# Performance work log

Hardware: AMD Instinct MI355X
Metric: run time of the kernel (lower is better)

The kernel has to match this reference:

```python
import jax, jax.numpy as jnp
import numpy as np

NUM_TOKENS = 8192
MODEL_DIM = 4096
NUM_EXPERTS = 64
CAPACITY_FACTOR = 1.0


def setup_inputs() -> dict:
    key = jax.random.key(0)
    k1, k2 = jax.random.split(key)
    inp = jax.random.normal(k1, (NUM_TOKENS, MODEL_DIM), dtype=jnp.float32)
    wg = jax.random.normal(k2, (NUM_EXPERTS, MODEL_DIM), dtype=jnp.float32) * (1.0 / np.sqrt(MODEL_DIM))
    return {"input": inp, "wg_weight": wg}


def reference(input, wg_weight):
    # logits = input @ wg.T  -> [T, E]
    logits = jnp.einsum('td,ed->te', input, wg_weight)
    num_tokens, num_experts = logits.shape
    capacity = int(CAPACITY_FACTOR * ((num_tokens + num_experts - 1) // num_experts))

    indices1_s = jnp.argmax(logits, axis=1)                      # [T]
    mask1 = jax.nn.one_hot(indices1_s, num_experts, dtype=logits.dtype)  # [T, E]
    gates = jax.nn.softmax(logits, axis=1)                       # [T, E]
    gates1_s = jnp.sum(gates * mask1, axis=1)                    # [T]

    # locations: position of each token within its chosen expert's queue
    # (exclusive cumsum over the one-hot mask, gathered at the chosen expert)
    locations1 = jnp.cumsum(mask1, axis=0) - 1.0                 # [T, E]
    locations1_s = jnp.sum(locations1 * mask1, axis=1).astype(jnp.int32)  # [T]

    # load-balancing aux loss (float32 branch of the original)
    me = jnp.sum(gates, axis=0)                                  # [E]
    ce = jnp.sum(mask1, axis=0)                                  # [E]
    l_aux = jnp.sum(me * ce) * (num_experts / (num_tokens * num_tokens))

    return (l_aux, indices1_s.astype(jnp.int32), locations1_s, gates1_s)
```

## Files before the change

### kernel.cpp

```cpp
#include <hip/hip_runtime.h>

namespace {
constexpr int TOK = 8192;
constexpr int DIM = 4096;
constexpr int NE  = 64;
constexpr int TB  = 128;
constexpr int KS  = 8;
constexpr int KR  = DIM / KS;
constexpr int NKS = KR / 32;
constexpr int TOTKS = DIM / 32;
constexpr int NT  = TOK / TB;
constexpr int GB  = 64;
constexpr int NCH = TOK / GB;
}

typedef _Float16 f16x8 __attribute__((ext_vector_type(8)));
typedef float    f32x4 __attribute__((ext_vector_type(4)));

__global__ __launch_bounds__(256) void prepack_w(
    const float* __restrict__ W, f16x8* __restrict__ whi,
    f16x8* __restrict__ wlo) {
  const int gid = blockIdx.x * 256 + threadIdx.x;
  const int lane = gid & 63;
  const int gk   = (gid >> 6) & (TOTKS - 1);
  const int et   = gid >> 13;
  const int e = et * 16 + (lane & 15);
  const int k = gk * 32 + (lane >> 4) * 8;
  const float4 r0 = *(const float4*)(W + (size_t)e * DIM + k);
  const float4 r1 = *(const float4*)(W + (size_t)e * DIM + k + 4);
  f16x8 hi, lo;
  const float rv[8] = {r0.x, r0.y, r0.z, r0.w, r1.x, r1.y, r1.z, r1.w};
#pragma unroll
  for (int j = 0; j < 8; ++j) {
    const _Float16 h = (_Float16)rv[j];
    hi[j] = h;
    lo[j] = (_Float16)(rv[j] - (float)h);
  }
  whi[gid] = hi;
  wlo[gid] = lo;
}

__global__ __launch_bounds__(512, 4) void gemm_split(
    const float* __restrict__ A, const f16x8* __restrict__ whi,
    const f16x8* __restrict__ wlo, float* __restrict__ partial) {
  const int bid  = blockIdx.x;
  const int tile = bid & (NT - 1);
  const int ks   = bid / NT;
  const int t0   = tile * TB;
  const int tid  = threadIdx.x;
  const int w    = tid >> 6;
  const int lane = tid & 63;
  const int col  = lane & 15;
  const int quad = lane >> 4;

  const float* Ap = A + (size_t)(t0 + w * 16 + col) * DIM + ks * KR + quad * 8;
  const int gk0 = ks * NKS;

  f32x4 acc[4];
#pragma unroll
  for (int et = 0; et < 4; ++et) acc[et] = (f32x4)0.0f;

  float4 a0  = *(const float4*)(Ap);
  float4 a1  = *(const float4*)(Ap + 4);
  float4 a0n = *(const float4*)(Ap + 32);
  float4 a1n = *(const float4*)(Ap + 36);
  f16x8 bh[4], bl[4];
#pragma unroll
  for (int et = 0; et < 4; ++et) {
    const size_t bi = ((size_t)(et * TOTKS + gk0) << 6) + lane;
    bh[et] = whi[bi];
    bl[et] = wlo[bi];
  }

  for (int it = 0; it < NKS; ++it) {
    f16x8 bhn[4], bln[4];
    if (it + 1 < NKS) {
#pragma unroll
      for (int et = 0; et < 4; ++et) {
        const size_t bi = ((size_t)(et * TOTKS + gk0 + it + 1) << 6) + lane;
        bhn[et] = whi[bi];
        bln[et] = wlo[bi];
      }
    }
    float4 a0nn, a1nn;
    if (it + 2 < NKS) {
      a0nn = *(const float4*)(Ap + (it + 2) * 32);
      a1nn = *(const float4*)(Ap + (it + 2) * 32 + 4);
    }
    const float av[8] = {a0.x, a0.y, a0.z, a0.w, a1.x, a1.y, a1.z, a1.w};
    f16x8 ah, al;
#pragma unroll
    for (int j = 0; j < 8; ++j) {
      const _Float16 h = (_Float16)av[j];
      ah[j] = h;
      al[j] = (_Float16)(av[j] - (float)h);
    }
#pragma unroll
    for (int et = 0; et < 4; ++et) {
      acc[et] = __builtin_amdgcn_mfma_f32_16x16x32_f16(ah, bh[et], acc[et], 0, 0, 0);
      acc[et] = __builtin_amdgcn_mfma_f32_16x16x32_f16(ah, bl[et], acc[et], 0, 0, 0);
      acc[et] = __builtin_amdgcn_mfma_f32_16x16x32_f16(al, bh[et], acc[et], 0, 0, 0);
    }
    a0 = a0n; a1 = a1n; a0n = a0nn; a1n = a1nn;
#pragma unroll
    for (int et = 0; et < 4; ++et) { bh[et] = bhn[et]; bl[et] = bln[et]; }
  }

  float* P = partial + (size_t)ks * TOK * NE;
  const int tb = t0 + w * 16 + quad * 4;
#pragma unroll
  for (int et = 0; et < 4; ++et) {
    const int e = et * 16 + col;
#pragma unroll
    for (int r = 0; r < 4; ++r)
      P[(size_t)(tb + r) * NE + e] = acc[et][r];
  }
}

__global__ __launch_bounds__(256) void gating(
    const float* __restrict__ partial, float* __restrict__ out,
    int* __restrict__ idx_int, int* __restrict__ rankp,
    int* __restrict__ hist, float* __restrict__ me_part) {
  __shared__ float L[GB * 65];
  __shared__ float mx[GB];
  __shared__ float dninv[GB];
  __shared__ int   eid[GB];
  const int b = blockIdx.x, tid = threadIdx.x;
  const size_t base = (size_t)b * GB * NE;

#pragma unroll
  for (int j = 0; j < (GB * NE) / 256; ++j) {
    const int idx = tid + 256 * j;
    float s = 0.0f;
#pragma unroll
    for (int k = 0; k < KS; ++k)
      s += partial[(size_t)k * TOK * NE + base + idx];
    L[(idx >> 6) * 65 + (idx & 63)] = s;
  }
  __syncthreads();

  if (tid < GB) {
    const int t = tid;
    float m = -3.0e38f; int bi = 0;
    for (int e = 0; e < NE; ++e) {
      const float v = L[t * 65 + e];
      if (v > m) { m = v; bi = e; }
    }
    float s = 0.0f;
    for (int e = 0; e < NE; ++e) s += __expf(L[t * 65 + e] - m);
    const float inv = 1.0f / s;
    mx[t] = m; dninv[t] = inv; eid[t] = bi;
    const int gt = b * GB + t;
    out[1 + gt]           = (float)bi;
    out[1 + 2 * TOK + gt] = inv;
    idx_int[gt] = bi;
  }
  __syncthreads();

  if (tid < GB) {
    const int t = tid, e = eid[t];
    int r = 0;
    for (int j = 0; j < t; ++j) r += (eid[j] == e) ? 1 : 0;
    rankp[b * GB + t] = r;
    int c = 0;
    for (int t2 = 0; t2 < GB; ++t2) c += (eid[t2] == tid) ? 1 : 0;
    hist[b * NE + tid] = c;
  } else if (tid < 2 * GB) {
    const int e = tid - GB;
    float s = 0.0f;
    for (int t2 = 0; t2 < GB; ++t2)
      s += __expf(L[t2 * 65 + e] - mx[t2]) * dninv[t2];
    me_part[b * NE + e] = s;
  }
}

__global__ __launch_bounds__(256) void finalize(
    const int* __restrict__ idx_int, const int* __restrict__ rankp,
    const int* __restrict__ hist, const float* __restrict__ me_part,
    float* __restrict__ out) {
  __shared__ int   H[NCH * NE];
  __shared__ int   SEG[4 * NE];
  __shared__ float MEp[4 * NE];
  __shared__ float CE[NE];
  const int tid = threadIdx.x;
  const int e = tid & 63, seg = tid >> 6;

  for (int j = tid; j < NCH * NE; j += 256) H[j] = hist[j];
  {
    float s = 0.0f;
    for (int c = seg * 32; c < seg * 32 + 32; ++c) s += me_part[c * NE + e];
    MEp[seg * NE + e] = s;
  }
  __syncthreads();
  {
    int hs = 0;
    for (int c = seg * 32; c < seg * 32 + 32; ++c) hs += H[c * NE + e];
    SEG[seg * NE + e] = hs;
  }
  __syncthreads();
  if (tid < NE) {
    int run = 0;
    for (int s2 = 0; s2 < 4; ++s2) {
      const int v = SEG[s2 * NE + tid];
      SEG[s2 * NE + tid] = run;
      run += v;
    }
    CE[tid] = (float)run;
  }
  __syncthreads();
  {
    int run = SEG[seg * NE + e];
    for (int c = seg * 32; c < seg * 32 + 32; ++c) {
      const int v = H[c * NE + e];
      H[c * NE + e] = run;
      run += v;
    }
  }
  if (tid < 64) {
    float p = (MEp[tid] + MEp[NE + tid] + MEp[2 * NE + tid] + MEp[3 * NE + tid])
              * CE[tid];
#pragma unroll
    for (int off = 32; off > 0; off >>= 1) p += __shfl_down(p, off);
    if (tid == 0) out[0] = p * ((float)NE / ((float)TOK * (float)TOK));
  }
  __syncthreads();
#pragma unroll 4
  for (int i = tid; i < TOK; i += 256) {
    const int ex = idx_int[i];
    out[1 + TOK + i] = (float)(H[(i >> 6) * NE + ex] + rankp[i]);
  }
}

extern "C" void kernel_launch(void* const* d_in, const int* in_sizes, int n_in,
                              void* d_out, int out_size, void* d_ws, size_t ws_size,
                              hipStream_t stream) {
  const float* A = (const float*)d_in[0];
  const float* W = (const float*)d_in[1];
  float* out = (float*)d_out;
  char* ws = (char*)d_ws;

  float* partial = (float*)ws;
  size_t off = (size_t)KS * TOK * NE * sizeof(float);
  f16x8* whi = (f16x8*)(ws + off);  off += (size_t)4 * TOTKS * 64 * 16;
  f16x8* wlo = (f16x8*)(ws + off);  off += (size_t)4 * TOTKS * 64 * 16;
  float* me_part = (float*)(ws + off);  off += (size_t)NCH * NE * sizeof(float);
  int* idx_int = (int*)(ws + off);      off += (size_t)TOK * sizeof(int);
  int* rankp   = (int*)(ws + off);      off += (size_t)TOK * sizeof(int);
  int* hist    = (int*)(ws + off);

  hipLaunchKernelGGL(prepack_w, dim3(128), dim3(256), 0, stream, W, whi, wlo);
  hipLaunchKernelGGL(gemm_split, dim3(NT * KS), dim3(512), 0, stream,
                     A, whi, wlo, partial);
  hipLaunchKernelGGL(gating, dim3(NCH), dim3(256), 0, stream, partial, out,
                     idx_int, rankp, hist, me_part);
  hipLaunchKernelGGL(finalize, dim3(1), dim3(256), 0, stream, idx_int, rankp,
                     hist, me_part, out);
}
```

Before: 220.4 us.

## Stage prepacked weight fragments in LDS via direct global-to-LDS loads

Each block of the split-K GEMM now cooperatively loads the hi/lo fp16 weight fragments for its K slice into shared memory with global_load_lds, in two halves, and all eight waves read them from LDS. Before, every wave fetched its own copy of the weights from global memory with register prefetching. The change cuts redundant global and L2 weight traffic by a factor of eight per block. In exchange it adds 64 KB of LDS per block, which may limit occupancy, plus block-wide barriers and the loss of the overlap that register prefetching gave.

Result: faster. 214.3 us (-2.8%).

```diff
diff --git a/kernel.cpp b/kernel.cpp
--- a/kernel.cpp
+++ b/kernel.cpp
@@ -41,8 +41,10 @@
 }
 
 __global__ __launch_bounds__(512, 4) void gemm_split(
-    const float* __restrict__ A, const f16x8* __restrict__ whi,
-    const f16x8* __restrict__ wlo, float* __restrict__ partial) {
+    const float* __restrict__ A, const _Float16* __restrict__ whi,
+    const _Float16* __restrict__ wlo, float* __restrict__ partial) {
+  __shared__ _Float16 sB[8 * 8 * 64 * 8];
+
   const int bid  = blockIdx.x;
   const int tile = bid & (NT - 1);
   const int ks   = bid / NT;
@@ -52,9 +54,9 @@
   const int lane = tid & 63;
   const int col  = lane & 15;
   const int quad = lane >> 4;
+  const int gk0  = ks * NKS;
 
   const float* Ap = A + (size_t)(t0 + w * 16 + col) * DIM + ks * KR + quad * 8;
-  const int gk0 = ks * NKS;
 
   f32x4 acc[4];
 #pragma unroll
@@ -64,46 +66,49 @@
   float4 a1  = *(const float4*)(Ap + 4);
   float4 a0n = *(const float4*)(Ap + 32);
   float4 a1n = *(const float4*)(Ap + 36);
-  f16x8 bh[4], bl[4];
-#pragma unroll
-  for (int et = 0; et < 4; ++et) {
-    const size_t bi = ((size_t)(et * TOTKS + gk0) << 6) + lane;
-    bh[et] = whi[bi];
-    bl[et] = wlo[bi];
-  }
-
-  for (int it = 0; it < NKS; ++it) {
-    f16x8 bhn[4], bln[4];
-    if (it + 1 < NKS) {
+
+  const _Float16* src_base =
+      ((w < 4) ? whi : wlo) + ((size_t)((w & 3) * TOTKS + gk0) << 9);
+  _Float16* dst_base = sB + ((size_t)w << 12);
+
+  for (int half = 0; half < 2; ++half) {
+    if (half) __syncthreads();
+#pragma unroll
+    for (int i = 0; i < 8; ++i) {
+      const _Float16* src = src_base + (((size_t)(half * 8 + i)) << 9) + lane * 8;
+      _Float16* dst = dst_base + ((size_t)i << 9) + lane * 8;
+      __builtin_amdgcn_global_load_lds(
+          (const __attribute__((address_space(1))) void*)src,
+          (__attribute__((address_space(3))) void*)dst, 16, 0, 0);
+    }
+    __syncthreads();
+
+    for (int s = 0; s < 8; ++s) {
+      const int it = half * 8 + s;
+      float4 a0nn, a1nn;
+      if (it + 2 < NKS) {
+        a0nn = *(const float4*)(Ap + (it + 2) * 32);
+        a1nn = *(const float4*)(Ap + (it + 2) * 32 + 4);
+      }
+      const float av[8] = {a0.x, a0.y, a0.z, a0.w, a1.x, a1.y, a1.z, a1.w};
+      f16x8 ah, al;
+#pragma unroll
+      for (int j = 0; j < 8; ++j) {
+        const _Float16 h = (_Float16)av[j];
+        ah[j] = h;
+        al[j] = (_Float16)(av[j] - (float)h);
+      }
 #pragma unroll
       for (int et = 0; et < 4; ++et) {
-        const size_t bi = ((size_t)(et * TOTKS + gk0 + it + 1) << 6) + lane;
-        bhn[et] = whi[bi];
-        bln[et] = wlo[bi];
+        const f16x8 bh = *(const f16x8*)(sB + ((et * 8 + s) << 9) + lane * 8);
+        const f16x8 bl =
+            *(const f16x8*)(sB + (((4 + et) * 8 + s) << 9) + lane * 8);
+        acc[et] = __builtin_amdgcn_mfma_f32_16x16x32_f16(ah, bh, acc[et], 0, 0, 0);
+        acc[et] = __builtin_amdgcn_mfma_f32_16x16x32_f16(ah, bl, acc[et], 0, 0, 0);
+        acc[et] = __builtin_amdgcn_mfma_f32_16x16x32_f16(al, bh, acc[et], 0, 0, 0);
       }
-    }
-    float4 a0nn, a1nn;
-    if (it + 2 < NKS) {
-      a0nn = *(const float4*)(Ap + (it + 2) * 32);
-      a1nn = *(const float4*)(Ap + (it + 2) * 32 + 4);
-    }
-    const float av[8] = {a0.x, a0.y, a0.z, a0.w, a1.x, a1.y, a1.z, a1.w};
-    f16x8 ah, al;
-#pragma unroll
-    for (int j = 0; j < 8; ++j) {
-      const _Float16 h = (_Float16)av[j];
-      ah[j] = h;
-      al[j] = (_Float16)(av[j] - (float)h);
-    }
-#pragma unroll
-    for (int et = 0; et < 4; ++et) {
-      acc[et] = __builtin_amdgcn_mfma_f32_16x16x32_f16(ah, bh[et], acc[et], 0, 0, 0);
-      acc[et] = __builtin_amdgcn_mfma_f32_16x16x32_f16(ah, bl[et], acc[et], 0, 0, 0);
-      acc[et] = __builtin_amdgcn_mfma_f32_16x16x32_f16(al, bh[et], acc[et], 0, 0, 0);
-    }
-    a0 = a0n; a1 = a1n; a0n = a0nn; a1n = a1nn;
-#pragma unroll
-    for (int et = 0; et < 4; ++et) { bh[et] = bhn[et]; bl[et] = bln[et]; }
+      a0 = a0n; a1 = a1n; a0n = a0nn; a1n = a1nn;
+    }
   }
 
   float* P = partial + (size_t)ks * TOK * NE;
@@ -241,14 +246,15 @@
 
   float* partial = (float*)ws;
   size_t off = (size_t)KS * TOK * NE * sizeof(float);
-  f16x8* whi = (f16x8*)(ws + off);  off += (size_t)4 * TOTKS * 64 * 16;
-  f16x8* wlo = (f16x8*)(ws + off);  off += (size_t)4 * TOTKS * 64 * 16;
+  _Float16* whi = (_Float16*)(ws + off);  off += (size_t)4 * TOTKS * 64 * 16;
+  _Float16* wlo = (_Float16*)(ws + off);  off += (size_t)4 * TOTKS * 64 * 16;
   float* me_part = (float*)(ws + off);  off += (size_t)NCH * NE * sizeof(float);
   int* idx_int = (int*)(ws + off);      off += (size_t)TOK * sizeof(int);
   int* rankp   = (int*)(ws + off);      off += (size_t)TOK * sizeof(int);
   int* hist    = (int*)(ws + off);
 
-  hipLaunchKernelGGL(prepack_w, dim3(128), dim3(256), 0, stream, W, whi, wlo);
+  hipLaunchKernelGGL(prepack_w, dim3(128), dim3(256), 0, stream, W,
+                     (f16x8*)whi, (f16x8*)wlo);
   hipLaunchKernelGGL(gemm_split, dim3(NT * KS), dim3(512), 0, stream,
                      A, whi, wlo, partial);
   hipLaunchKernelGGL(gating, dim3(NCH), dim3(256), 0, stream, partial, out,
```
